# Optimization experiments

Measured on AMD Instinct MI355X. Metric: run time of the kernel, lower is better.

## Reference

```python
import jax, jax.numpy as jnp
import numpy as np

B, D, H, E, K = 8192, 1024, 256, 16, 4


def setup_inputs() -> dict:
    key = jax.random.key(0)
    ks = jax.random.split(key, 6)
    s_d = D ** -0.5
    s_h = H ** -0.5
    return {
        "x": jax.random.normal(ks[0], (B, D), dtype=jnp.float32),
        "route_w": jax.random.normal(ks[1], (E, D), dtype=jnp.float32) * s_d,
        "w1": jax.random.normal(ks[2], (E, H, D), dtype=jnp.float32) * s_d,
        "b1": jax.random.normal(ks[3], (E, H), dtype=jnp.float32) * s_d,
        "w2": jax.random.normal(ks[4], (E, D, H), dtype=jnp.float32) * s_h,
        "b2": jax.random.normal(ks[5], (E, D), dtype=jnp.float32) * s_h,
    }


def _moe_forward(x, route_w, w1, b1, w2, b2):
    # Router: logits (B, E) -> top-k softmax weights scattered back to (B, E).
    logits = x @ route_w.T
    top_vals, top_idx = jax.lax.top_k(logits, K)
    top_w = jax.nn.softmax(top_vals, axis=-1)
    rows = jnp.arange(x.shape[0])[:, None]
    weights = jnp.zeros_like(logits).at[rows, top_idx].set(top_w)  # (B, E)

    # Experts: out = sum_e w[:, e] * relu(relu(x W1e^T + b1e) W2e^T + b2e)
    # Non-selected experts have weight 0, so dense-then-weight matches the
    # original masked gather/scatter math exactly (dropout = 0).
    def step(out, params_e):
        W1, bb1, W2, bb2, we = params_e
        h = jax.nn.relu(x @ W1.T + bb1)       # (B, H)
        y = jax.nn.relu(h @ W2.T + bb2)       # (B, D)
        return out + y * we[:, None], None

    out0 = jnp.zeros_like(x)
    out, _ = jax.lax.scan(step, out0, (w1, b1, w2, b2, weights.T))
    return out


def reference(x, route_w, w1, b1, w2, b2):
    return _moe_forward(x, route_w, w1, b1, w2, b2)
```

## Files before the change

### kernel.cpp

```cpp
#include <hip/hip_runtime.h>
#include <stdint.h>

typedef unsigned short u16;
typedef __attribute__((ext_vector_type(8))) short bf16x8;
typedef __attribute__((ext_vector_type(4))) float f32x4;
typedef __attribute__((ext_vector_type(8))) u16 u16x8;
typedef __attribute__((ext_vector_type(4))) u16 u16x4;

#define NTOK 8192
#define DDIM 1024
#define HDIM 256
#define NEXP 16
#define MAXT 272
#define MAXSLOT (MAXT * 128)

__device__ __forceinline__ u16 f2bf(float f) {
  uint32_t u = __builtin_bit_cast(uint32_t, f);
  u += 0x7FFFu + ((u >> 16) & 1u);
  return (u16)(u >> 16);
}
__device__ __forceinline__ float bf2f(u16 h) {
  return __builtin_bit_cast(float, (uint32_t)h << 16);
}

__device__ __forceinline__ void gll16(const void* g, void* l) {
  __builtin_amdgcn_global_load_lds((const __attribute__((address_space(1))) void*)g,
                                   (__attribute__((address_space(3))) void*)l,
                                   16, 0, 0);
}

__global__ __launch_bounds__(256) void cvt2_kernel(const float* __restrict__ a,
                                                   const float* __restrict__ b,
                                                   u16* __restrict__ oa,
                                                   u16* __restrict__ ob,
                                                   int nba) {
  const float* in; u16* out;
  int bx = blockIdx.x;
  if (bx < nba) { in = a; out = oa; } else { in = b; out = ob; bx -= nba; }
  size_t i = ((size_t)bx * 256 + threadIdx.x) * 8;
  const float4 p = *(const float4*)(in + i);
  const float4 q = *(const float4*)(in + i + 4);
  u16x8 o;
  o[0] = f2bf(p.x); o[1] = f2bf(p.y); o[2] = f2bf(p.z); o[3] = f2bf(p.w);
  o[4] = f2bf(q.x); o[5] = f2bf(q.y); o[6] = f2bf(q.z); o[7] = f2bf(q.w);
  *(u16x8*)(out + i) = o;
}

__global__ __launch_bounds__(256) void zero_out_kernel(float* __restrict__ p) {
  size_t i = ((size_t)blockIdx.x * 256 + threadIdx.x) * 4;
  *(float4*)(p + i) = (float4){0.f, 0.f, 0.f, 0.f};
}

__global__ __launch_bounds__(256) void router_kernel(const float* __restrict__ x,
                                                     const float* __restrict__ rw,
                                                     int* __restrict__ epack,
                                                     float* __restrict__ ew,
                                                     u16* __restrict__ xbf) {
  __shared__ __align__(16) uint8_t rwlds[65536];
  const int tid = threadIdx.x;

#pragma unroll
  for (int i = 0; i < 16; ++i) {
    int byte = (i * 256 + tid) * 16;
    int sw = byte ^ (((byte >> 8) & 7) << 4);
    *(float4*)(rwlds + sw) = *(const float4*)((const uint8_t*)rw + byte);
  }
  __syncthreads();

  const int lane = tid & 63, wid = tid >> 6;
  const int s = lane & 15;
  const int tok = blockIdx.x * 16 + wid * 4 + (lane >> 4);
  const float* xrow = x + (size_t)tok * DDIM;
  u16* xbrow = xbf + (size_t)tok * DDIM;

  double acc[NEXP];
#pragma unroll
  for (int e = 0; e < NEXP; ++e) acc[e] = 0.0;

#pragma unroll 4
  for (int g = 0; g < 16; ++g) {
    const int d = s * 64 + g * 4;
    float4 xv = *(const float4*)(xrow + d);
    u16x4 o;
    o[0] = f2bf(xv.x); o[1] = f2bf(xv.y); o[2] = f2bf(xv.z); o[3] = f2bf(xv.w);
    *(u16x4*)(xbrow + d) = o;
    const double x0 = xv.x, x1 = xv.y, x2 = xv.z, x3 = xv.w;
    const int roff = (s * 256 + g * 16) ^ ((s & 7) << 4);
#pragma unroll
    for (int e = 0; e < NEXP; ++e) {
      float4 rv = *(const float4*)(rwlds + e * 4096 + roff);
      acc[e] = fma(x0, (double)rv.x, acc[e]);
      acc[e] = fma(x1, (double)rv.y, acc[e]);
      acc[e] = fma(x2, (double)rv.z, acc[e]);
      acc[e] = fma(x3, (double)rv.w, acc[e]);
    }
  }

#define FOLD(H, M)                                                   \
  _Pragma("unroll") for (int i = 0; i < H; ++i) {                    \
    double send = (lane & M) ? acc[i] : acc[i + H];                  \
    double recv = __shfl_xor(send, M);                               \
    acc[i] = ((lane & M) ? acc[i + H] : acc[i]) + recv;              \
  }
  FOLD(8, 1)
  FOLD(4, 2)
  FOLD(2, 4)
  FOLD(1, 8)
#undef FOLD
  const int e_mine = ((lane & 1) << 3) | ((lane & 2) << 1) |
                     ((lane & 4) >> 1) | ((lane & 8) >> 3);

  double val = acc[0];
  double tv[4]; int tidx[4];
#pragma unroll
  for (int k = 0; k < 4; ++k) {
    double bv = val; int be = e_mine;
#pragma unroll
    for (int m = 1; m < 16; m <<= 1) {
      double ov = __shfl_xor(bv, m);
      int oe = __shfl_xor(be, m);
      if (ov > bv || (ov == bv && oe < be)) { bv = ov; be = oe; }
    }
    tv[k] = bv; tidx[k] = be;
    if (e_mine == be) val = -1.0e300;
  }

  if ((lane & 15) == 0) {
    float m0 = (float)tv[0];
    float w[4]; float sum = 0.f;
#pragma unroll
    for (int k = 0; k < 4; ++k) { w[k] = expf((float)tv[k] - m0); sum += w[k]; }
    epack[tok] = tidx[0] | (tidx[1] << 8) | (tidx[2] << 16) | (tidx[3] << 24);
#pragma unroll
    for (int k = 0; k < 4; ++k) ew[tok * 4 + k] = w[k] / sum;
  }
}

__global__ __launch_bounds__(1024) void compact_kernel(const int* __restrict__ epack,
                                                       const float* __restrict__ ew,
                                                       int* __restrict__ texp,
                                                       int* __restrict__ perm,
                                                       float* __restrict__ wsl,
                                                       int* __restrict__ islot) {
  __shared__ int wave_cnt[16][NEXP];
  __shared__ int counts_sm[NEXP];
  __shared__ int wtot[16], wave_off[16];
  const int e = blockIdx.x;
  const int tid = threadIdx.x, lane = tid & 63, w = tid >> 6;

  int ep[8]; unsigned m[8];
#pragma unroll
  for (int j = 0; j < 8; ++j) {
    ep[j] = epack[tid * 8 + j];
    m[j] = (1u << (ep[j] & 255)) | (1u << ((ep[j] >> 8) & 255)) |
           (1u << ((ep[j] >> 16) & 255)) | (1u << ((ep[j] >> 24) & 255));
  }
#pragma unroll
  for (int ee = 0; ee < NEXP; ++ee) {
    int c = 0;
#pragma unroll
    for (int j = 0; j < 8; ++j) c += (m[j] >> ee) & 1u;
#pragma unroll
    for (int off = 32; off > 0; off >>= 1) c += __shfl_xor(c, off);
    if (lane == 0) wave_cnt[w][ee] = c;
  }
  unsigned fm = 0;
#pragma unroll
  for (int j = 0; j < 8; ++j) fm |= ((m[j] >> e) & 1u) << j;
  int s = __popc(fm);
  int incl = s;
#pragma unroll
  for (int d = 1; d < 64; d <<= 1) {
    int t2 = __shfl_up(incl, d);
    if (lane >= d) incl += t2;
  }
  if (lane == 63) wtot[w] = incl;
  __syncthreads();
  if (tid < NEXP) {
    int c = 0;
    for (int w2 = 0; w2 < 16; ++w2) c += wave_cnt[w2][tid];
    counts_sm[tid] = c;
  }
  if (tid == 0) {
    int run = 0;
    for (int w2 = 0; w2 < 16; ++w2) { wave_off[w2] = run; run += wtot[w2]; }
  }
  __syncthreads();
  int base = 0;
  for (int ee = 0; ee < NEXP; ++ee)
    if (ee < e) base += ((counts_sm[ee] + 127) >> 7) << 7;
  int pos = base + wave_off[w] + (incl - s);
#pragma unroll
  for (int j = 0; j < 8; ++j) {
    if ((fm >> j) & 1u) {
      int tok = tid * 8 + j;
      int b0 = ep[j] & 255, b1 = (ep[j] >> 8) & 255, b2_ = (ep[j] >> 16) & 255;
      int k = (b0 == e) ? 0 : ((b1 == e) ? 1 : ((b2_ == e) ? 2 : 3));
      perm[pos] = tok;
      wsl[pos] = ew[tok * 4 + k];
      islot[tok * 4 + k] = pos;
      ++pos;
    }
  }
  int cnt = counts_sm[e];
  int pad = (((cnt + 127) >> 7) << 7) - cnt;
  if (tid < pad) { perm[base + cnt + tid] = 0; wsl[base + cnt + tid] = 0.f; }
  if (e == 0 && tid == 0) {
    int tc = 0;
    for (int ee = 0; ee < NEXP; ++ee) {
      int nt = (counts_sm[ee] + 127) >> 7;
      for (int i = 0; i < nt; ++i) texp[tc++] = ee;
    }
    for (; tc < MAXT; ++tc) texp[tc] = -1;
  }
}

__device__ __forceinline__ void stage128w(const u16* __restrict__ base, int ld,
                                          int kbase, uint8_t* dst, int tid) {
#pragma unroll
  for (int i = 0; i < 2; ++i) {
    int u = i * 512 + tid;
    int row = u >> 3, g = u & 7;
    gll16(base + (size_t)row * ld + kbase + ((g ^ (row & 7)) << 3), dst + u * 16);
  }
}
__device__ __forceinline__ void gather128w(const u16* __restrict__ xbf,
                                           const int tok[2], int kbase,
                                           uint8_t* dst, int tid) {
#pragma unroll
  for (int i = 0; i < 2; ++i) {
    int u = i * 512 + tid;
    int g = u & 7;
    gll16(xbf + (size_t)tok[i] * DDIM + kbase + ((g ^ ((u >> 3) & 7)) << 3), dst + u * 16);
  }
}

__device__ __forceinline__ void mma32x64(const uint8_t* Ab, const uint8_t* Bb,
                                         f32x4 acc[2][4], int wm, int wn,
                                         int lrow, int lk) {
#pragma unroll
  for (int s = 0; s < 2; ++s) {
    bf16x8 af[2], bfr[4];
#pragma unroll
    for (int f = 0; f < 2; ++f) {
      int ar = wm * 32 + f * 16 + lrow;
      af[f] = *(const bf16x8*)(Ab + ar * 128 + ((((s << 2) | lk) ^ (ar & 7)) << 4));
    }
#pragma unroll
    for (int f = 0; f < 4; ++f) {
      int br = wn * 64 + f * 16 + lrow;
      bfr[f] = *(const bf16x8*)(Bb + br * 128 + ((((s << 2) | lk) ^ (br & 7)) << 4));
    }
#pragma unroll
    for (int i = 0; i < 2; ++i)
#pragma unroll
      for (int j = 0; j < 4; ++j)
        acc[i][j] = __builtin_amdgcn_mfma_f32_16x16x32_bf16(af[i], bfr[j], acc[i][j], 0, 0, 0);
  }
}

__global__ __launch_bounds__(512) void gemm1_kernel(const u16* __restrict__ xbf,
                                                    const u16* __restrict__ w1bf,
                                                    const float* __restrict__ b1,
                                                    const int* __restrict__ texp,
                                                    const int* __restrict__ perm,
                                                    u16* __restrict__ Hc, int t0) {
  __shared__ __align__(16) uint8_t smem[2][32768];
  const int t = t0 + blockIdx.x;
  const int e = (t < MAXT) ? texp[t] : -1;
  if (e < 0) return;
  const int n0 = blockIdx.y * 128;
  const int tid = threadIdx.x;
  const int lane = tid & 63, wid = tid >> 6;
  const int wm = wid >> 1, wn = wid & 1;
  const int lrow = lane & 15, lk = lane >> 4;

  int tok[2];
#pragma unroll
  for (int i = 0; i < 2; ++i) tok[i] = perm[t * 128 + ((i * 512 + tid) >> 3)];
  const u16* Bsrc = w1bf + ((size_t)e * HDIM + n0) * DDIM;

  f32x4 acc[2][4];
#pragma unroll
  for (int i = 0; i < 2; ++i)
#pragma unroll
    for (int j = 0; j < 4; ++j) acc[i][j] = (f32x4){0.f, 0.f, 0.f, 0.f};

  gather128w(xbf, tok, 0, smem[0], tid);
  stage128w(Bsrc, DDIM, 0, smem[0] + 16384, tid);
  __syncthreads();
  int cur = 0;
  for (int kt = 0; kt < 16; ++kt) {
    if (kt < 15) {
      gather128w(xbf, tok, (kt + 1) * 64, smem[cur ^ 1], tid);
      stage128w(Bsrc, DDIM, (kt + 1) * 64, smem[cur ^ 1] + 16384, tid);
    }
    mma32x64(smem[cur], smem[cur] + 16384, acc, wm, wn, lrow, lk);
    __syncthreads();
    cur ^= 1;
  }
#pragma unroll
  for (int j = 0; j < 4; ++j) {
    int n = n0 + wn * 64 + j * 16 + lrow;
    float bias = b1[e * HDIM + n];
#pragma unroll
    for (int i = 0; i < 2; ++i) {
      int rloc = (t - t0) * 128 + wm * 32 + i * 16 + lk * 4;
#pragma unroll
      for (int r = 0; r < 4; ++r) {
        float h = fmaxf(acc[i][j][r] + bias, 0.f);
        Hc[((size_t)rloc + r) * HDIM + n] = f2bf(h);
      }
    }
  }
}

__global__ __launch_bounds__(512) void gemm2_main_kernel(const u16* __restrict__ Hc,
                                                         const u16* __restrict__ w2bf,
                                                         const float* __restrict__ b2,
                                                         const int* __restrict__ texp,
                                                         u16* __restrict__ ybuf,
                                                         int nbase, int NC) {
  __shared__ __align__(16) uint8_t smem[2][32768];
  const int t = blockIdx.x;
  const int e = texp[t];
  if (e < 0) return;
  const int nl0 = blockIdx.y * 128;
  const int tid = threadIdx.x;
  const int lane = tid & 63, wid = tid >> 6;
  const int wm = wid >> 1, wn = wid & 1;
  const int lrow = lane & 15, lk = lane >> 4;

  const u16* Asrc = Hc + (size_t)t * 128 * HDIM;
  const u16* Bsrc = w2bf + ((size_t)e * DDIM + nbase + nl0) * HDIM;

  f32x4 acc[2][4];
#pragma unroll
  for (int i = 0; i < 2; ++i)
#pragma unroll
    for (int j = 0; j < 4; ++j) acc[i][j] = (f32x4){0.f, 0.f, 0.f, 0.f};

  stage128w(Asrc, HDIM, 0, smem[0], tid);
  stage128w(Bsrc, HDIM, 0, smem[0] + 16384, tid);
  __syncthreads();
  int cur = 0;
  for (int kt = 0; kt < 4; ++kt) {
    if (kt < 3) {
      stage128w(Asrc, HDIM, (kt + 1) * 64, smem[cur ^ 1], tid);
      stage128w(Bsrc, HDIM, (kt + 1) * 64, smem[cur ^ 1] + 16384, tid);
    }
    mma32x64(smem[cur], smem[cur] + 16384, acc, wm, wn, lrow, lk);
    __syncthreads();
    cur ^= 1;
  }
  float bias[4];
#pragma unroll
  for (int j = 0; j < 4; ++j)
    bias[j] = b2[e * DDIM + nbase + nl0 + wn * 64 + j * 16 + lrow];
#pragma unroll
  for (int i = 0; i < 2; ++i) {
#pragma unroll
    for (int r = 0; r < 4; ++r) {
      int slot = t * 128 + wm * 32 + i * 16 + lk * 4 + r;
#pragma unroll
      for (int j = 0; j < 4; ++j) {
        int nloc = nl0 + wn * 64 + j * 16 + lrow;
        float h = fmaxf(acc[i][j][r] + bias[j], 0.f);
        ybuf[(size_t)slot * NC + nloc] = f2bf(h);
      }
    }
  }
}

__global__ __launch_bounds__(512) void gemm2_fb_kernel(const u16* __restrict__ Hc,
                                                       const u16* __restrict__ w2bf,
                                                       const float* __restrict__ b2,
                                                       const int* __restrict__ texp,
                                                       const int* __restrict__ perm,
                                                       const float* __restrict__ wsl,
                                                       float* __restrict__ out, int t0) {
  __shared__ __align__(16) uint8_t smem[2][32768];
  const int t = t0 + blockIdx.x;
  const int e = (t < MAXT) ? texp[t] : -1;
  if (e < 0) return;
  const int nl0 = blockIdx.y * 128;
  const int tid = threadIdx.x;
  const int lane = tid & 63, wid = tid >> 6;
  const int wm = wid >> 1, wn = wid & 1;
  const int lrow = lane & 15, lk = lane >> 4;

  const u16* Asrc = Hc + (size_t)(t - t0) * 128 * HDIM;
  const u16* Bsrc = w2bf + ((size_t)e * DDIM + nl0) * HDIM;

  f32x4 acc[2][4];
#pragma unroll
  for (int i = 0; i < 2; ++i)
#pragma unroll
    for (int j = 0; j < 4; ++j) acc[i][j] = (f32x4){0.f, 0.f, 0.f, 0.f};

  stage128w(Asrc, HDIM, 0, smem[0], tid);
  stage128w(Bsrc, HDIM, 0, smem[0] + 16384, tid);
  __syncthreads();
  int cur = 0;
  for (int kt = 0; kt < 4; ++kt) {
    if (kt < 3) {
      stage128w(Asrc, HDIM, (kt + 1) * 64, smem[cur ^ 1], tid);
      stage128w(Bsrc, HDIM, (kt + 1) * 64, smem[cur ^ 1] + 16384, tid);
    }
    mma32x64(smem[cur], smem[cur] + 16384, acc, wm, wn, lrow, lk);
    __syncthreads();
    cur ^= 1;
  }
  float bias[4];
#pragma unroll
  for (int j = 0; j < 4; ++j)
    bias[j] = b2[e * DDIM + nl0 + wn * 64 + j * 16 + lrow];
#pragma unroll
  for (int i = 0; i < 2; ++i) {
#pragma unroll
    for (int r = 0; r < 4; ++r) {
      int slot = t * 128 + wm * 32 + i * 16 + lk * 4 + r;
      int tokn = perm[slot];
      float w = wsl[slot];
#pragma unroll
      for (int j = 0; j < 4; ++j) {
        int n = nl0 + wn * 64 + j * 16 + lrow;
        float h = fmaxf(acc[i][j][r] + bias[j], 0.f);
        atomicAdd(&out[(size_t)tokn * DDIM + n], w * h);
      }
    }
  }
}

__global__ __launch_bounds__(256) void combine_kernel(const u16* __restrict__ ybuf,
                                                      const float* __restrict__ ew,
                                                      const int* __restrict__ islot,
                                                      float* __restrict__ out,
                                                      int n0, int NC, int cshift) {
  int gid = blockIdx.x * 256 + threadIdx.x;
  int t = gid >> cshift;
  int c = (gid & ((1 << cshift) - 1)) << 2;
  const int4 sl = *(const int4*)(islot + t * 4);
  const float4 w = *(const float4*)(ew + t * 4);
  float4 a = {0.f, 0.f, 0.f, 0.f};
#define ACC(SL, W)                                             \
  {                                                            \
    u16x4 y = *(const u16x4*)(ybuf + (size_t)(SL)*NC + c);     \
    a.x += (W)*bf2f(y[0]); a.y += (W)*bf2f(y[1]);              \
    a.z += (W)*bf2f(y[2]); a.w += (W)*bf2f(y[3]);              \
  }
  ACC(sl.x, w.x); ACC(sl.y, w.y); ACC(sl.z, w.z); ACC(sl.w, w.w);
#undef ACC
  *(float4*)(out + (size_t)t * DDIM + n0 + c) = a;
}

extern "C" void kernel_launch(void* const* d_in, const int* in_sizes, int n_in,
                              void* d_out, int out_size, void* d_ws, size_t ws_size,
                              hipStream_t stream) {
  const float* x = (const float*)d_in[0];
  const float* route_w = (const float*)d_in[1];
  const float* w1 = (const float*)d_in[2];
  const float* b1 = (const float*)d_in[3];
  const float* w2 = (const float*)d_in[4];
  const float* b2 = (const float*)d_in[5];
  float* out = (float*)d_out;

  uint8_t* ws = (uint8_t*)d_ws;
  const size_t OFF_EPACK = 0;
  const size_t OFF_EW    = 32768;
  const size_t OFF_ISLOT = 163840;
  const size_t OFF_TEXP  = 294912;
  const size_t OFF_PERM  = 296960;
  const size_t OFF_WSL   = 436224;
  const size_t OFF_X     = 1048576;
  const size_t OFF_W1    = OFF_X + (size_t)NTOK * DDIM * 2;
  const size_t OFF_W2    = OFF_W1 + (size_t)NEXP * HDIM * DDIM * 2;
  const size_t OFF_HC    = OFF_W2 + (size_t)NEXP * DDIM * HDIM * 2;
  const size_t OFF_Y     = OFF_HC + (size_t)MAXSLOT * HDIM * 2;

  int* epack  = (int*)(ws + OFF_EPACK);
  float* ew   = (float*)(ws + OFF_EW);
  int* islot  = (int*)(ws + OFF_ISLOT);
  int* texp   = (int*)(ws + OFF_TEXP);
  int* perm   = (int*)(ws + OFF_PERM);
  float* wsl  = (float*)(ws + OFF_WSL);
  u16* xbf    = (u16*)(ws + OFF_X);
  u16* w1bf   = (u16*)(ws + OFF_W1);
  u16* w2bf   = (u16*)(ws + OFF_W2);
  u16* Hc     = (u16*)(ws + OFF_HC);
  u16* ybuf   = (u16*)(ws + OFF_Y);

  const int nba = (NEXP * HDIM * DDIM) / 2048;
  cvt2_kernel<<<dim3(nba * 2), 256, 0, stream>>>(w1, w2, w1bf, w2bf, nba);
  router_kernel<<<dim3(NTOK / 16), 256, 0, stream>>>(x, route_w, epack, ew, xbf);
  compact_kernel<<<dim3(NEXP), 1024, 0, stream>>>(epack, ew, texp, perm, wsl, islot);

  int ybN = 0;
  for (int cand = 1024; cand >= 128; cand >>= 1) {
    if (ws_size >= OFF_Y + (size_t)MAXSLOT * cand * 2) { ybN = cand; break; }
  }

  if (ybN > 0) {
    gemm1_kernel<<<dim3(MAXT, HDIM / 128), 512, 0, stream>>>(xbf, w1bf, b1, texp, perm, Hc, 0);
    int cshift = __builtin_ctz(ybN >> 2);
    for (int nb = 0; nb < DDIM; nb += ybN) {
      gemm2_main_kernel<<<dim3(MAXT, ybN / 128), 512, 0, stream>>>(
          Hc, w2bf, b2, texp, ybuf, nb, ybN);
      combine_kernel<<<dim3((NTOK << cshift) / 256), 256, 0, stream>>>(
          ybuf, ew, islot, out, nb, ybN, cshift);
    }
  } else {
    long room = (long)ws_size - (long)OFF_HC;
    int CT = (int)(room / 65536);
    if (CT > MAXT) CT = MAXT;
    if (CT < 16) CT = 16;
    zero_out_kernel<<<dim3((NTOK * DDIM) / 1024), 256, 0, stream>>>(out);
    for (int t0 = 0; t0 < MAXT; t0 += CT) {
      int ct = (MAXT - t0 < CT) ? (MAXT - t0) : CT;
      gemm1_kernel<<<dim3(ct, HDIM / 128), 512, 0, stream>>>(
          xbf, w1bf, b1, texp, perm, Hc, t0);
      gemm2_fb_kernel<<<dim3(ct, DDIM / 128), 512, 0, stream>>>(
          Hc, w2bf, b2, texp, perm, wsl, out, t0);
    }
  }
}
```

Before: 141.0 us.

## Stage GEMM epilogues through LDS, widen gemm2 N-tile, vectorize combine

The gemm1 and gemm2 epilogues now write their bf16 results into swizzled shared memory first and then copy them out with 16-byte coalesced stores, replacing scattered 2-byte global stores. gemm2_main now computes two 128-column chunks per block, so each block reuses its staged A tile across 256 output columns and half as many blocks are launched. The combine kernel handles 16 columns per thread with 16-byte loads. The costs are extra syncs and more accumulator registers in gemm2, and the smallest workspace fallback size is raised from 128 to 256 columns.

```diff
diff --git a/kernel.cpp b/kernel.cpp
--- a/kernel.cpp
+++ b/kernel.cpp
@@ -259,6 +259,23 @@
   }
 }
 
+__device__ __forceinline__ void epi_store(u16* olds, const f32x4 acc[2][4],
+                                          const float bias[4], int wm, int wn,
+                                          int lrow, int lk) {
+#pragma unroll
+  for (int i = 0; i < 2; ++i)
+#pragma unroll
+    for (int r = 0; r < 4; ++r) {
+      int row = wm * 32 + i * 16 + lk * 4 + r;
+#pragma unroll
+      for (int j = 0; j < 4; ++j) {
+        int col = wn * 64 + j * 16 + lrow;
+        float h = fmaxf(acc[i][j][r] + bias[j], 0.f);
+        olds[row * 128 + (col ^ ((row & 15) << 3))] = f2bf(h);
+      }
+    }
+}
+
 __global__ __launch_bounds__(512) void gemm1_kernel(const u16* __restrict__ xbf,
                                                     const u16* __restrict__ w1bf,
                                                     const float* __restrict__ b1,
@@ -299,19 +316,18 @@
     __syncthreads();
     cur ^= 1;
   }
-#pragma unroll
-  for (int j = 0; j < 4; ++j) {
-    int n = n0 + wn * 64 + j * 16 + lrow;
-    float bias = b1[e * HDIM + n];
-#pragma unroll
-    for (int i = 0; i < 2; ++i) {
-      int rloc = (t - t0) * 128 + wm * 32 + i * 16 + lk * 4;
-#pragma unroll
-      for (int r = 0; r < 4; ++r) {
-        float h = fmaxf(acc[i][j][r] + bias, 0.f);
-        Hc[((size_t)rloc + r) * HDIM + n] = f2bf(h);
-      }
-    }
+  u16* olds = (u16*)smem;
+  float bias[4];
+#pragma unroll
+  for (int j = 0; j < 4; ++j) bias[j] = b1[e * HDIM + n0 + wn * 64 + j * 16 + lrow];
+  epi_store(olds, acc, bias, wm, wn, lrow, lk);
+  __syncthreads();
+#pragma unroll
+  for (int i2 = 0; i2 < 4; ++i2) {
+    int u = i2 * 512 + tid;
+    int row = u >> 4, col = (u & 15) * 8;
+    u16x8 v = *(const u16x8*)(olds + row * 128 + (col ^ ((row & 15) << 3)));
+    *(u16x8*)(Hc + ((size_t)(t - t0) * 128 + row) * HDIM + n0 + col) = v;
   }
 }
 
@@ -325,7 +341,7 @@
   const int t = blockIdx.x;
   const int e = texp[t];
   if (e < 0) return;
-  const int nl0 = blockIdx.y * 128;
+  const int nl0 = blockIdx.y * 256;
   const int tid = threadIdx.x;
   const int lane = tid & 63, wid = tid >> 6;
   const int wm = wid >> 1, wn = wid & 1;
@@ -334,41 +350,48 @@
   const u16* Asrc = Hc + (size_t)t * 128 * HDIM;
   const u16* Bsrc = w2bf + ((size_t)e * DDIM + nbase + nl0) * HDIM;
 
-  f32x4 acc[2][4];
-#pragma unroll
-  for (int i = 0; i < 2; ++i)
-#pragma unroll
-    for (int j = 0; j < 4; ++j) acc[i][j] = (f32x4){0.f, 0.f, 0.f, 0.f};
+  f32x4 acc[2][2][4];
+#pragma unroll
+  for (int nc = 0; nc < 2; ++nc)
+#pragma unroll
+    for (int i = 0; i < 2; ++i)
+#pragma unroll
+      for (int j = 0; j < 4; ++j) acc[nc][i][j] = (f32x4){0.f, 0.f, 0.f, 0.f};
 
   stage128w(Asrc, HDIM, 0, smem[0], tid);
   stage128w(Bsrc, HDIM, 0, smem[0] + 16384, tid);
   __syncthreads();
   int cur = 0;
-  for (int kt = 0; kt < 4; ++kt) {
-    if (kt < 3) {
-      stage128w(Asrc, HDIM, (kt + 1) * 64, smem[cur ^ 1], tid);
-      stage128w(Bsrc, HDIM, (kt + 1) * 64, smem[cur ^ 1] + 16384, tid);
-    }
-    mma32x64(smem[cur], smem[cur] + 16384, acc, wm, wn, lrow, lk);
+#pragma unroll
+  for (int s = 0; s < 8; ++s) {
+    const int nc = s >> 2;
+    if (s < 7) {
+      const int kt2 = (s + 1) & 3, nc2 = (s + 1) >> 2;
+      stage128w(Asrc, HDIM, kt2 * 64, smem[cur ^ 1], tid);
+      stage128w(Bsrc + (size_t)(nc2 * 128) * HDIM, HDIM, kt2 * 64,
+                smem[cur ^ 1] + 16384, tid);
+    }
+    mma32x64(smem[cur], smem[cur] + 16384, acc[nc], wm, wn, lrow, lk);
     __syncthreads();
     cur ^= 1;
   }
-  float bias[4];
-#pragma unroll
-  for (int j = 0; j < 4; ++j)
-    bias[j] = b2[e * DDIM + nbase + nl0 + wn * 64 + j * 16 + lrow];
-#pragma unroll
-  for (int i = 0; i < 2; ++i) {
-#pragma unroll
-    for (int r = 0; r < 4; ++r) {
-      int slot = t * 128 + wm * 32 + i * 16 + lk * 4 + r;
-#pragma unroll
-      for (int j = 0; j < 4; ++j) {
-        int nloc = nl0 + wn * 64 + j * 16 + lrow;
-        float h = fmaxf(acc[i][j][r] + bias[j], 0.f);
-        ybuf[(size_t)slot * NC + nloc] = f2bf(h);
-      }
-    }
+  u16* olds = (u16*)smem;
+#pragma unroll
+  for (int nc = 0; nc < 2; ++nc) {
+    float bias[4];
+#pragma unroll
+    for (int j = 0; j < 4; ++j)
+      bias[j] = b2[e * DDIM + nbase + nl0 + nc * 128 + wn * 64 + j * 16 + lrow];
+    epi_store(olds, acc[nc], bias, wm, wn, lrow, lk);
+    __syncthreads();
+#pragma unroll
+    for (int i2 = 0; i2 < 4; ++i2) {
+      int u = i2 * 512 + tid;
+      int row = u >> 4, col = (u & 15) * 8;
+      u16x8 v = *(const u16x8*)(olds + row * 128 + (col ^ ((row & 15) << 3)));
+      *(u16x8*)(ybuf + (size_t)(t * 128 + row) * NC + nl0 + nc * 128 + col) = v;
+    }
+    __syncthreads();
   }
 }
 
@@ -439,19 +462,26 @@
                                                       int n0, int NC, int cshift) {
   int gid = blockIdx.x * 256 + threadIdx.x;
   int t = gid >> cshift;
-  int c = (gid & ((1 << cshift) - 1)) << 2;
+  int c = (gid & ((1 << cshift) - 1)) << 4;
   const int4 sl = *(const int4*)(islot + t * 4);
   const float4 w = *(const float4*)(ew + t * 4);
-  float4 a = {0.f, 0.f, 0.f, 0.f};
-#define ACC(SL, W)                                             \
-  {                                                            \
-    u16x4 y = *(const u16x4*)(ybuf + (size_t)(SL)*NC + c);     \
-    a.x += (W)*bf2f(y[0]); a.y += (W)*bf2f(y[1]);              \
-    a.z += (W)*bf2f(y[2]); a.w += (W)*bf2f(y[3]);              \
-  }
-  ACC(sl.x, w.x); ACC(sl.y, w.y); ACC(sl.z, w.z); ACC(sl.w, w.w);
-#undef ACC
-  *(float4*)(out + (size_t)t * DDIM + n0 + c) = a;
+  float a[16];
+#pragma unroll
+  for (int k = 0; k < 16; ++k) a[k] = 0.f;
+#define ACCROW(SL, W)                                                      \
+  {                                                                        \
+    u16x8 y0 = *(const u16x8*)(ybuf + (size_t)(SL)*NC + c);                \
+    u16x8 y1 = *(const u16x8*)(ybuf + (size_t)(SL)*NC + c + 8);            \
+    _Pragma("unroll") for (int k = 0; k < 8; ++k) {                        \
+      a[k] += (W)*bf2f(y0[k]); a[8 + k] += (W)*bf2f(y1[k]);                \
+    }                                                                      \
+  }
+  ACCROW(sl.x, w.x); ACCROW(sl.y, w.y); ACCROW(sl.z, w.z); ACCROW(sl.w, w.w);
+#undef ACCROW
+  float* o = out + (size_t)t * DDIM + n0 + c;
+#pragma unroll
+  for (int k = 0; k < 16; k += 4)
+    *(float4*)(o + k) = (float4){a[k], a[k + 1], a[k + 2], a[k + 3]};
 }
 
 extern "C" void kernel_launch(void* const* d_in, const int* in_sizes, int n_in,
@@ -496,15 +526,15 @@
   compact_kernel<<<dim3(NEXP), 1024, 0, stream>>>(epack, ew, texp, perm, wsl, islot);
 
   int ybN = 0;
-  for (int cand = 1024; cand >= 128; cand >>= 1) {
+  for (int cand = 1024; cand >= 256; cand >>= 1) {
     if (ws_size >= OFF_Y + (size_t)MAXSLOT * cand * 2) { ybN = cand; break; }
   }
 
   if (ybN > 0) {
     gemm1_kernel<<<dim3(MAXT, HDIM / 128), 512, 0, stream>>>(xbf, w1bf, b1, texp, perm, Hc, 0);
-    int cshift = __builtin_ctz(ybN >> 2);
+    int cshift = __builtin_ctz(ybN >> 4);
     for (int nb = 0; nb < DDIM; nb += ybN) {
-      gemm2_main_kernel<<<dim3(MAXT, ybN / 128), 512, 0, stream>>>(
+      gemm2_main_kernel<<<dim3(MAXT, ybN / 256), 512, 0, stream>>>(
           Hc, w2bf, b2, texp, ybuf, nb, ybN);
       combine_kernel<<<dim3((NTOK << cshift) / 256), 256, 0, stream>>>(
           ybuf, ew, islot, out, nb, ybN, cshift);
```

Measured after the change: 155.9 us. 1.11x slower.

## Load GEMM A operand directly to registers, halve LDS, widen combine

Applied to the files above, without the earlier changes.

Both GEMM kernels now load the activation (A) fragments straight from global memory into registers per wave, instead of staging them through shared memory. Only the weight tile is double-buffered in LDS, which halves LDS use per block, and launch bounds request more resident blocks. The combine kernel now processes 16 columns per thread with wider loads. The risks are exposed global load latency for the A fragments, since they are not prefetched ahead, and register pressure from the occupancy hint.

```diff
diff --git a/kernel.cpp b/kernel.cpp
--- a/kernel.cpp
+++ b/kernel.cpp
@@ -224,28 +224,12 @@
     gll16(base + (size_t)row * ld + kbase + ((g ^ (row & 7)) << 3), dst + u * 16);
   }
 }
-__device__ __forceinline__ void gather128w(const u16* __restrict__ xbf,
-                                           const int tok[2], int kbase,
-                                           uint8_t* dst, int tid) {
-#pragma unroll
-  for (int i = 0; i < 2; ++i) {
-    int u = i * 512 + tid;
-    int g = u & 7;
-    gll16(xbf + (size_t)tok[i] * DDIM + kbase + ((g ^ ((u >> 3) & 7)) << 3), dst + u * 16);
-  }
-}
-
-__device__ __forceinline__ void mma32x64(const uint8_t* Ab, const uint8_t* Bb,
-                                         f32x4 acc[2][4], int wm, int wn,
-                                         int lrow, int lk) {
+
+__device__ __forceinline__ void mma_areg(const bf16x8 a[2][2], const uint8_t* Bb,
+                                         f32x4 acc[2][4], int wn, int lrow, int lk) {
 #pragma unroll
   for (int s = 0; s < 2; ++s) {
-    bf16x8 af[2], bfr[4];
-#pragma unroll
-    for (int f = 0; f < 2; ++f) {
-      int ar = wm * 32 + f * 16 + lrow;
-      af[f] = *(const bf16x8*)(Ab + ar * 128 + ((((s << 2) | lk) ^ (ar & 7)) << 4));
-    }
+    bf16x8 bfr[4];
 #pragma unroll
     for (int f = 0; f < 4; ++f) {
       int br = wn * 64 + f * 16 + lrow;
@@ -255,17 +239,17 @@
     for (int i = 0; i < 2; ++i)
 #pragma unroll
       for (int j = 0; j < 4; ++j)
-        acc[i][j] = __builtin_amdgcn_mfma_f32_16x16x32_bf16(af[i], bfr[j], acc[i][j], 0, 0, 0);
-  }
-}
-
-__global__ __launch_bounds__(512) void gemm1_kernel(const u16* __restrict__ xbf,
-                                                    const u16* __restrict__ w1bf,
-                                                    const float* __restrict__ b1,
-                                                    const int* __restrict__ texp,
-                                                    const int* __restrict__ perm,
-                                                    u16* __restrict__ Hc, int t0) {
-  __shared__ __align__(16) uint8_t smem[2][32768];
+        acc[i][j] = __builtin_amdgcn_mfma_f32_16x16x32_bf16(a[i][s], bfr[j], acc[i][j], 0, 0, 0);
+  }
+}
+
+__global__ __launch_bounds__(512, 6) void gemm1_kernel(const u16* __restrict__ xbf,
+                                                       const u16* __restrict__ w1bf,
+                                                       const float* __restrict__ b1,
+                                                       const int* __restrict__ texp,
+                                                       const int* __restrict__ perm,
+                                                       u16* __restrict__ Hc, int t0) {
+  __shared__ __align__(16) uint8_t bsm[2][16384];
   const int t = t0 + blockIdx.x;
   const int e = (t < MAXT) ? texp[t] : -1;
   if (e < 0) return;
@@ -275,9 +259,8 @@
   const int wm = wid >> 1, wn = wid & 1;
   const int lrow = lane & 15, lk = lane >> 4;
 
-  int tok[2];
-#pragma unroll
-  for (int i = 0; i < 2; ++i) tok[i] = perm[t * 128 + ((i * 512 + tid) >> 3)];
+  const u16* arow0 = xbf + (size_t)perm[t * 128 + wm * 32 + lrow] * DDIM;
+  const u16* arow1 = xbf + (size_t)perm[t * 128 + wm * 32 + 16 + lrow] * DDIM;
   const u16* Bsrc = w1bf + ((size_t)e * HDIM + n0) * DDIM;
 
   f32x4 acc[2][4];
@@ -286,16 +269,18 @@
 #pragma unroll
     for (int j = 0; j < 4; ++j) acc[i][j] = (f32x4){0.f, 0.f, 0.f, 0.f};
 
-  gather128w(xbf, tok, 0, smem[0], tid);
-  stage128w(Bsrc, DDIM, 0, smem[0] + 16384, tid);
+  stage128w(Bsrc, DDIM, 0, bsm[0], tid);
   __syncthreads();
   int cur = 0;
+#pragma unroll
   for (int kt = 0; kt < 16; ++kt) {
-    if (kt < 15) {
-      gather128w(xbf, tok, (kt + 1) * 64, smem[cur ^ 1], tid);
-      stage128w(Bsrc, DDIM, (kt + 1) * 64, smem[cur ^ 1] + 16384, tid);
-    }
-    mma32x64(smem[cur], smem[cur] + 16384, acc, wm, wn, lrow, lk);
+    if (kt < 15) stage128w(Bsrc, DDIM, (kt + 1) * 64, bsm[cur ^ 1], tid);
+    bf16x8 a[2][2];
+    a[0][0] = *(const bf16x8*)(arow0 + kt * 64 + lk * 8);
+    a[0][1] = *(const bf16x8*)(arow0 + kt * 64 + 32 + lk * 8);
+    a[1][0] = *(const bf16x8*)(arow1 + kt * 64 + lk * 8);
+    a[1][1] = *(const bf16x8*)(arow1 + kt * 64 + 32 + lk * 8);
+    mma_areg(a, bsm[cur], acc, wn, lrow, lk);
     __syncthreads();
     cur ^= 1;
   }
@@ -315,13 +300,13 @@
   }
 }
 
-__global__ __launch_bounds__(512) void gemm2_main_kernel(const u16* __restrict__ Hc,
-                                                         const u16* __restrict__ w2bf,
-                                                         const float* __restrict__ b2,
-                                                         const int* __restrict__ texp,
-                                                         u16* __restrict__ ybuf,
-                                                         int nbase, int NC) {
-  __shared__ __align__(16) uint8_t smem[2][32768];
+__global__ __launch_bounds__(512, 6) void gemm2_main_kernel(const u16* __restrict__ Hc,
+                                                            const u16* __restrict__ w2bf,
+                                                            const float* __restrict__ b2,
+                                                            const int* __restrict__ texp,
+                                                            u16* __restrict__ ybuf,
+                                                            int nbase, int NC) {
+  __shared__ __align__(16) uint8_t bsm[2][16384];
   const int t = blockIdx.x;
   const int e = texp[t];
   if (e < 0) return;
@@ -331,7 +316,8 @@
   const int wm = wid >> 1, wn = wid & 1;
   const int lrow = lane & 15, lk = lane >> 4;
 
-  const u16* Asrc = Hc + (size_t)t * 128 * HDIM;
+  const u16* arow0 = Hc + ((size_t)t * 128 + wm * 32 + lrow) * HDIM;
+  const u16* arow1 = arow0 + 16 * HDIM;
   const u16* Bsrc = w2bf + ((size_t)e * DDIM + nbase + nl0) * HDIM;
 
   f32x4 acc[2][4];
@@ -340,16 +326,18 @@
 #pragma unroll
     for (int j = 0; j < 4; ++j) acc[i][j] = (f32x4){0.f, 0.f, 0.f, 0.f};
 
-  stage128w(Asrc, HDIM, 0, smem[0], tid);
-  stage128w(Bsrc, HDIM, 0, smem[0] + 16384, tid);
+  stage128w(Bsrc, HDIM, 0, bsm[0], tid);
   __syncthreads();
   int cur = 0;
+#pragma unroll
   for (int kt = 0; kt < 4; ++kt) {
-    if (kt < 3) {
-      stage128w(Asrc, HDIM, (kt + 1) * 64, smem[cur ^ 1], tid);
-      stage128w(Bsrc, HDIM, (kt + 1) * 64, smem[cur ^ 1] + 16384, tid);
-    }
-    mma32x64(smem[cur], smem[cur] + 16384, acc, wm, wn, lrow, lk);
+    if (kt < 3) stage128w(Bsrc, HDIM, (kt + 1) * 64, bsm[cur ^ 1], tid);
+    bf16x8 a[2][2];
+    a[0][0] = *(const bf16x8*)(arow0 + kt * 64 + lk * 8);
+    a[0][1] = *(const bf16x8*)(arow0 + kt * 64 + 32 + lk * 8);
+    a[1][0] = *(const bf16x8*)(arow1 + kt * 64 + lk * 8);
+    a[1][1] = *(const bf16x8*)(arow1 + kt * 64 + 32 + lk * 8);
+    mma_areg(a, bsm[cur], acc, wn, lrow, lk);
     __syncthreads();
     cur ^= 1;
   }
@@ -372,14 +360,14 @@
   }
 }
 
-__global__ __launch_bounds__(512) void gemm2_fb_kernel(const u16* __restrict__ Hc,
-                                                       const u16* __restrict__ w2bf,
-                                                       const float* __restrict__ b2,
-                                                       const int* __restrict__ texp,
-                                                       const int* __restrict__ perm,
-                                                       const float* __restrict__ wsl,
-                                                       float* __restrict__ out, int t0) {
-  __shared__ __align__(16) uint8_t smem[2][32768];
+__global__ __launch_bounds__(512, 6) void gemm2_fb_kernel(const u16* __restrict__ Hc,
+                                                          const u16* __restrict__ w2bf,
+                                                          const float* __restrict__ b2,
+                                                          const int* __restrict__ texp,
+                                                          const int* __restrict__ perm,
+                                                          const float* __restrict__ wsl,
+                                                          float* __restrict__ out, int t0) {
+  __shared__ __align__(16) uint8_t bsm[2][16384];
   const int t = t0 + blockIdx.x;
   const int e = (t < MAXT) ? texp[t] : -1;
   if (e < 0) return;
@@ -389,7 +377,8 @@
   const int wm = wid >> 1, wn = wid & 1;
   const int lrow = lane & 15, lk = lane >> 4;
 
-  const u16* Asrc = Hc + (size_t)(t - t0) * 128 * HDIM;
+  const u16* arow0 = Hc + ((size_t)(t - t0) * 128 + wm * 32 + lrow) * HDIM;
+  const u16* arow1 = arow0 + 16 * HDIM;
   const u16* Bsrc = w2bf + ((size_t)e * DDIM + nl0) * HDIM;
 
   f32x4 acc[2][4];
@@ -398,16 +387,18 @@
 #pragma unroll
     for (int j = 0; j < 4; ++j) acc[i][j] = (f32x4){0.f, 0.f, 0.f, 0.f};
 
-  stage128w(Asrc, HDIM, 0, smem[0], tid);
-  stage128w(Bsrc, HDIM, 0, smem[0] + 16384, tid);
+  stage128w(Bsrc, HDIM, 0, bsm[0], tid);
   __syncthreads();
   int cur = 0;
+#pragma unroll
   for (int kt = 0; kt < 4; ++kt) {
-    if (kt < 3) {
-      stage128w(Asrc, HDIM, (kt + 1) * 64, smem[cur ^ 1], tid);
-      stage128w(Bsrc, HDIM, (kt + 1) * 64, smem[cur ^ 1] + 16384, tid);
-    }
-    mma32x64(smem[cur], smem[cur] + 16384, acc, wm, wn, lrow, lk);
+    if (kt < 3) stage128w(Bsrc, HDIM, (kt + 1) * 64, bsm[cur ^ 1], tid);
+    bf16x8 a[2][2];
+    a[0][0] = *(const bf16x8*)(arow0 + kt * 64 + lk * 8);
+    a[0][1] = *(const bf16x8*)(arow0 + kt * 64 + 32 + lk * 8);
+    a[1][0] = *(const bf16x8*)(arow1 + kt * 64 + lk * 8);
+    a[1][1] = *(const bf16x8*)(arow1 + kt * 64 + 32 + lk * 8);
+    mma_areg(a, bsm[cur], acc, wn, lrow, lk);
     __syncthreads();
     cur ^= 1;
   }
@@ -439,19 +430,26 @@
                                                       int n0, int NC, int cshift) {
   int gid = blockIdx.x * 256 + threadIdx.x;
   int t = gid >> cshift;
-  int c = (gid & ((1 << cshift) - 1)) << 2;
+  int c = (gid & ((1 << cshift) - 1)) << 4;
   const int4 sl = *(const int4*)(islot + t * 4);
   const float4 w = *(const float4*)(ew + t * 4);
-  float4 a = {0.f, 0.f, 0.f, 0.f};
-#define ACC(SL, W)                                             \
-  {                                                            \
-    u16x4 y = *(const u16x4*)(ybuf + (size_t)(SL)*NC + c);     \
-    a.x += (W)*bf2f(y[0]); a.y += (W)*bf2f(y[1]);              \
-    a.z += (W)*bf2f(y[2]); a.w += (W)*bf2f(y[3]);              \
-  }
-  ACC(sl.x, w.x); ACC(sl.y, w.y); ACC(sl.z, w.z); ACC(sl.w, w.w);
-#undef ACC
-  *(float4*)(out + (size_t)t * DDIM + n0 + c) = a;
+  float a[16];
+#pragma unroll
+  for (int k = 0; k < 16; ++k) a[k] = 0.f;
+#define ACCROW(SL, W)                                                      \
+  {                                                                        \
+    u16x8 y0 = *(const u16x8*)(ybuf + (size_t)(SL)*NC + c);                \
+    u16x8 y1 = *(const u16x8*)(ybuf + (size_t)(SL)*NC + c + 8);            \
+    _Pragma("unroll") for (int k = 0; k < 8; ++k) {                        \
+      a[k] += (W)*bf2f(y0[k]); a[8 + k] += (W)*bf2f(y1[k]);                \
+    }                                                                      \
+  }
+  ACCROW(sl.x, w.x); ACCROW(sl.y, w.y); ACCROW(sl.z, w.z); ACCROW(sl.w, w.w);
+#undef ACCROW
+  float* o = out + (size_t)t * DDIM + n0 + c;
+#pragma unroll
+  for (int k = 0; k < 16; k += 4)
+    *(float4*)(o + k) = (float4){a[k], a[k + 1], a[k + 2], a[k + 3]};
 }
 
 extern "C" void kernel_launch(void* const* d_in, const int* in_sizes, int n_in,
@@ -502,7 +500,7 @@
 
   if (ybN > 0) {
     gemm1_kernel<<<dim3(MAXT, HDIM / 128), 512, 0, stream>>>(xbf, w1bf, b1, texp, perm, Hc, 0);
-    int cshift = __builtin_ctz(ybN >> 2);
+    int cshift = __builtin_ctz(ybN >> 4);
     for (int nb = 0; nb < DDIM; nb += ybN) {
       gemm2_main_kernel<<<dim3(MAXT, ybN / 128), 512, 0, stream>>>(
           Hc, w2bf, b2, texp, ybuf, nb, ybN);
```

New measurement: 187.4 us. +32.9%, slower.
